# Optimization experiments

Hardware: AMD Instinct MI355X
Metric: run time of the kernel (lower is better)

## Reference

```python
import jax, jax.numpy as jnp
import numpy as np

S, B, DIN = 3, 4096, 1024
H1, H2, H3, D = 512, 384, 256, 128
K, C = 512, 3            # codebook size, n_codebooks
TEMP = 0.1               # contrastive temperature
EPS = 1e-12


def setup_inputs() -> dict:
    key = jax.random.key(0)
    ks = jax.random.split(key, 16)
    g = lambda k, shp, s=0.05: (jax.random.normal(k, shp, dtype=jnp.float32) * s)
    return {
        'x': jax.random.normal(ks[0], (S, B, DIN), dtype=jnp.float32),
        'enc_w1': g(ks[1], (S, DIN, H1)), 'enc_b1': g(ks[2], (S, H1)),
        'enc_w2': g(ks[3], (S, H1, H2)), 'enc_b2': g(ks[4], (S, H2)),
        'enc_w3': g(ks[5], (S, H2, H3)), 'enc_b3': g(ks[6], (S, H3)),
        'enc_w4': g(ks[7], (S, H3, D)),  'enc_b4': g(ks[8], (S, D)),
        'q_w1': g(ks[9], (D, D)), 'q_b1': g(ks[10], (D,)),
        'q_w2': g(ks[11], (D,)),
        'codebooks': jax.random.normal(ks[12], (C, K, D), dtype=jnp.float32),
    }


def _normalize(v):
    return v / jnp.maximum(jnp.linalg.norm(v, axis=-1, keepdims=True), EPS)


def _forward(x, enc_w1, enc_b1, enc_w2, enc_b2, enc_w3, enc_b3,
             enc_w4, enc_b4, q_w1, q_b1, q_w2, codebooks):
    sg = jax.lax.stop_gradient
    # per-source MLP encoders (stacked over source axis s)
    h = jax.nn.relu(jnp.einsum('sbi,sio->sbo', x, enc_w1) + enc_b1[:, None, :])
    h = jax.nn.relu(jnp.einsum('sbi,sio->sbo', h, enc_w2) + enc_b2[:, None, :])
    h = jax.nn.relu(jnp.einsum('sbi,sio->sbo', h, enc_w3) + enc_b3[:, None, :])
    emb = jnp.einsum('sbi,sio->sbo', h, enc_w4) + enc_b4[:, None, :]  # [S,B,D]

    # attention fusion: Linear->Tanh->Linear(1) per source, softmax over sources
    score = jnp.einsum('sbd,d->sb', jnp.tanh(jnp.einsum('sbd,de->sbe', emb, q_w1) + q_b1), q_w2)
    weight = jax.nn.softmax(score.T, axis=-1)                # [B,S]
    fused = jnp.einsum('bs,sbd->bd', weight, emb)            # [B,D]

    # residual VQ over C codebooks (straight-through, MSE losses)
    res = fused
    q_sum = jnp.zeros_like(fused)
    commit_loss = jnp.float32(0.0)
    for k in range(C):
        e = codebooks[k]                                     # [K,D]
        d2 = (jnp.sum(res * res, axis=1, keepdims=True)
              - 2.0 * res @ e.T + jnp.sum(e * e, axis=1))    # [B,K]
        ids = jnp.argmin(d2, axis=1)
        q = e[ids]                                           # [B,D]
        commit_loss = commit_loss + jnp.mean((sg(q) - res) ** 2)
        q_st = res + sg(q - res)                             # straight-through
        q_sum = q_sum + q_st
        res = res - q_st

    # codebook regularizer: mean pairwise cosine gram of normalized codebooks
    cbn = _normalize(codebooks)
    codebook_loss = jnp.mean(jnp.einsum('mkd,mjd->mkj', cbn, cbn))

    # contrastive losses (projection = identity)
    z1 = _normalize(q_sum)                                   # [B,D]
    contrast = []
    for s in range(S):
        z2 = _normalize(emb[s])
        refl = jnp.exp((z1 @ z1.T) / TEMP)                   # [B,B]
        between = jnp.exp((z1 @ z2.T) / TEMP)
        pos = jnp.diagonal(between)
        denom = refl.sum(1) + between.sum(1) - jnp.diagonal(refl)
        contrast.append(jnp.mean(-jnp.log(pos / denom)))

    return jnp.stack([1.0 * codebook_loss, 0.0 * commit_loss] + contrast)


def reference(x, enc_w1, enc_b1, enc_w2, enc_b2, enc_w3, enc_b3,
              enc_w4, enc_b4, q_w1, q_b1, q_w2, codebooks):
    return _forward(x, enc_w1, enc_b1, enc_w2, enc_b2, enc_w3, enc_b3,
                    enc_w4, enc_b4, q_w1, q_b1, q_w2, codebooks)
```

## Files before the change

### kernel.cpp

```cpp
#include <hip/hip_runtime.h>
#include <hip/hip_bf16.h>

#define S_   3
#define B_   4096
#define DIN_ 1024
#define H1_  512
#define H2_  384
#define H3_  256
#define D_   128
#define K_   512
#define C_   3
#define INV_T 10.0f
#define EPS_  1e-12f
#define EXP10 22026.465794806718f

typedef float f32x4 __attribute__((ext_vector_type(4)));
typedef short bf16x8 __attribute__((ext_vector_type(8)));

__device__ __forceinline__ unsigned short f2bf(float f) {
  unsigned int u = __float_as_uint(f);
  u = (u + 0x7FFF + ((u >> 16) & 1)) >> 16;
  return (unsigned short)u;
}

__device__ __forceinline__ float waveReduceSum(float v) {
#pragma unroll
  for (int off = 32; off > 0; off >>= 1) v += __shfl_down(v, off, 64);
  return v;
}

__device__ __forceinline__ float waveXorSum(float v) {
#pragma unroll
  for (int off = 32; off > 0; off >>= 1) v += __shfl_xor(v, off, 64);
  return v;
}

__device__ __forceinline__ float blockReduceSum128(float v, float* sbuf) {
  v = waveReduceSum(v);
  if ((threadIdx.x & 63) == 0) sbuf[threadIdx.x >> 6] = v;
  __syncthreads();
  float r = sbuf[0] + sbuf[1];
  __syncthreads();
  return r;
}

__global__ __launch_bounds__(256) void cvt_bf16_kernel(const float* __restrict__ in,
                                                       unsigned short* __restrict__ out,
                                                       int n) {
  int i = (blockIdx.x * 256 + threadIdx.x) * 4;
  if (i < n) {
    float4 v = *(const float4*)(in + i);
    out[i + 0] = f2bf(v.x); out[i + 1] = f2bf(v.y);
    out[i + 2] = f2bf(v.z); out[i + 3] = f2bf(v.w);
  }
}

__global__ __launch_bounds__(256) void transpose_w_kernel(const float* __restrict__ W,
                                                          unsigned short* __restrict__ Wt,
                                                          int K, int N) {
  const int s = blockIdx.z;
  const int k0 = blockIdx.x * 32, n0 = blockIdx.y * 32;
  const int tx = threadIdx.x, ty = threadIdx.y;
  __shared__ float t[32][33];
  const float* Ws = W + (size_t)s * K * N;
  unsigned short* Wts = Wt + (size_t)s * N * K;
#pragma unroll
  for (int i = 0; i < 4; i++)
    t[ty + 8 * i][tx] = Ws[(size_t)(k0 + ty + 8 * i) * N + n0 + tx];
  __syncthreads();
#pragma unroll
  for (int i = 0; i < 4; i++)
    Wts[(size_t)(n0 + ty + 8 * i) * K + k0 + tx] = f2bf(t[tx][ty + 8 * i]);
}

__global__ __launch_bounds__(256) void gemm_lds_kernel(
    const unsigned short* __restrict__ A, const unsigned short* __restrict__ Wt,
    const float* __restrict__ bias, void* __restrict__ Y,
    int K, int N, int relu, int out_f32) {
  const int t = threadIdx.x;
  const int lane = t & 63;
  const int w = t >> 6;
  const int ln = lane & 15, q = lane >> 4;
  const int wm = w >> 1, wn = w & 1;
  const int n0 = blockIdx.x * 128;
  const int mblk = blockIdx.y;
  const int s = mblk >> 6;
  const int m0 = mblk * 64;

  const unsigned short* Ag = A + (size_t)m0 * K;
  const unsigned short* Bg = Wt + (size_t)s * N * K + (size_t)n0 * K;
  const float* bs = bias + (size_t)s * N;

  __shared__ unsigned short Asm[2 * 64 * 32];
  __shared__ unsigned short Bsm[2 * 128 * 32];

  const int arow0 = t >> 3, ak8 = t & 7;
  const int aL0 = (ak8 >> 2) * 2048 + arow0 * 32 + (ak8 & 3) * 8;
  const int bL0 = (ak8 >> 2) * 4096 + arow0 * 32 + (ak8 & 3) * 8;
  const size_t gA0 = (size_t)arow0 * K + ak8 * 8;

  bf16x8 ra0 = *(const bf16x8*)(Ag + gA0);
  bf16x8 ra1 = *(const bf16x8*)(Ag + gA0 + (size_t)32 * K);
  bf16x8 rb0 = *(const bf16x8*)(Bg + gA0);
  bf16x8 rb1 = *(const bf16x8*)(Bg + gA0 + (size_t)32 * K);
  bf16x8 rb2 = *(const bf16x8*)(Bg + gA0 + (size_t)64 * K);
  bf16x8 rb3 = *(const bf16x8*)(Bg + gA0 + (size_t)96 * K);

  f32x4 acc[2][4];
#pragma unroll
  for (int i = 0; i < 2; i++)
#pragma unroll
    for (int j = 0; j < 4; j++) acc[i][j] = (f32x4){0.f, 0.f, 0.f, 0.f};

  for (int k0 = 0; k0 < K; k0 += 64) {
    *(bf16x8*)&Asm[aL0] = ra0;
    *(bf16x8*)&Asm[aL0 + 1024] = ra1;
    *(bf16x8*)&Bsm[bL0] = rb0;
    *(bf16x8*)&Bsm[bL0 + 1024] = rb1;
    *(bf16x8*)&Bsm[bL0 + 2048] = rb2;
    *(bf16x8*)&Bsm[bL0 + 3072] = rb3;
    __syncthreads();
    if (k0 + 64 < K) {
      const size_t g = gA0 + k0 + 64;
      ra0 = *(const bf16x8*)(Ag + g);
      ra1 = *(const bf16x8*)(Ag + g + (size_t)32 * K);
      rb0 = *(const bf16x8*)(Bg + g);
      rb1 = *(const bf16x8*)(Bg + g + (size_t)32 * K);
      rb2 = *(const bf16x8*)(Bg + g + (size_t)64 * K);
      rb3 = *(const bf16x8*)(Bg + g + (size_t)96 * K);
    }
    bf16x8 af[2][2], bf[4][2];
#pragma unroll
    for (int ti = 0; ti < 2; ti++)
#pragma unroll
      for (int ksl = 0; ksl < 2; ksl++)
        af[ti][ksl] = *(const bf16x8*)&Asm[ksl * 2048 + (wm * 32 + ti * 16 + ln) * 32 + q * 8];
#pragma unroll
    for (int tj = 0; tj < 4; tj++)
#pragma unroll
      for (int ksl = 0; ksl < 2; ksl++)
        bf[tj][ksl] = *(const bf16x8*)&Bsm[ksl * 4096 + (wn * 64 + tj * 16 + ln) * 32 + q * 8];
#pragma unroll
    for (int ksl = 0; ksl < 2; ksl++)
#pragma unroll
      for (int ti = 0; ti < 2; ti++)
#pragma unroll
        for (int tj = 0; tj < 4; tj++)
          acc[ti][tj] = __builtin_amdgcn_mfma_f32_16x16x32_bf16(af[ti][ksl], bf[tj][ksl], acc[ti][tj], 0, 0, 0);
    __syncthreads();
  }

#pragma unroll
  for (int ti = 0; ti < 2; ti++)
#pragma unroll
    for (int tj = 0; tj < 4; tj++) {
      const int cc = n0 + wn * 64 + tj * 16 + ln;
      const float bv = bs[cc];
#pragma unroll
      for (int reg = 0; reg < 4; reg++) {
        const int r = m0 + wm * 32 + ti * 16 + q * 4 + reg;
        float v = acc[ti][tj][reg] + bv;
        if (relu) v = fmaxf(v, 0.0f);
        if (out_f32) ((float*)Y)[(size_t)r * N + cc] = v;
        else ((unsigned short*)Y)[(size_t)r * N + cc] = f2bf(v);
      }
    }
}

__global__ __launch_bounds__(256) void score_kernel(
    const float* __restrict__ emb, const float* __restrict__ qw1,
    const float* __restrict__ qb1, const float* __restrict__ qw2,
    float* __restrict__ score) {
  const int b0 = blockIdx.x * 4;
  const int t = threadIdx.x;
  const int g = t >> 7, d = t & 127;
  __shared__ float e[12][D_];
  __shared__ float red[4][6];
#pragma unroll
  for (int i = 0; i < 3; i++) {
    int idx = i * 512 + t * 2;
    int r = idx >> 7, dd = idx & 127;
    int s = r >> 2, bi = r & 3;
    *(float2*)&e[r][dd] = *(const float2*)(emb + ((size_t)(s * B_ + b0 + bi)) * D_ + dd);
  }
  __syncthreads();
  float acc[6] = {0.f, 0.f, 0.f, 0.f, 0.f, 0.f};
  for (int i = 0; i < D_; i++) {
    float w = qw1[i * D_ + d];
#pragma unroll
    for (int j = 0; j < 6; j++) acc[j] = fmaf(e[g * 6 + j][i], w, acc[j]);
  }
  const float qb = qb1[d], q2 = qw2[d];
  float val[6];
#pragma unroll
  for (int j = 0; j < 6; j++) val[j] = tanhf(acc[j] + qb) * q2;
  const int wave = t >> 6;
#pragma unroll
  for (int j = 0; j < 6; j++) {
    float v = waveReduceSum(val[j]);
    if ((t & 63) == 0) red[wave][j] = v;
  }
  __syncthreads();
  if (t < 12) {
    int gg = t / 6, j = t % 6;
    int r = gg * 6 + j;
    int s = r >> 2, bi = r & 3;
    score[s * B_ + b0 + bi] = red[2 * gg][j] + red[2 * gg + 1][j];
  }
}

__global__ __launch_bounds__(128) void fuse_kernel(
    const float* __restrict__ emb, const float* __restrict__ score,
    float* __restrict__ fused) {
  const int b = blockIdx.x, d = threadIdx.x;
  float s0 = score[0 * B_ + b], s1 = score[1 * B_ + b], s2 = score[2 * B_ + b];
  float mx = fmaxf(s0, fmaxf(s1, s2));
  float e0 = __expf(s0 - mx), e1 = __expf(s1 - mx), e2 = __expf(s2 - mx);
  float inv = 1.0f / (e0 + e1 + e2);
  fused[(long long)b * D_ + d] =
      e0 * inv * emb[(long long)(0 * B_ + b) * D_ + d] +
      e1 * inv * emb[(long long)(1 * B_ + b) * D_ + d] +
      e2 * inv * emb[(long long)(2 * B_ + b) * D_ + d];
}

__global__ __launch_bounds__(64) void cbnorm2_kernel(const float* __restrict__ cb,
                                                     float* __restrict__ cbn2) {
  const int r = blockIdx.x, lane = threadIdx.x;
  const float* row = cb + (long long)r * D_;
  float v0 = row[lane], v1 = row[lane + 64];
  float t = waveReduceSum(v0 * v0 + v1 * v1);
  if (lane == 0) cbn2[r] = t;
}

__global__ __launch_bounds__(512) void vq_mfma_kernel(
    const float* __restrict__ fused, const float* __restrict__ cb,
    const unsigned short* __restrict__ cbb, const float* __restrict__ cbn2,
    float* __restrict__ qsum) {
  const int r0 = blockIdx.x * 16;
  const int t = threadIdx.x;
  const int w = t >> 6, lane = t & 63;
  const int ln = lane & 15, q = lane >> 4;
  __shared__ float resv[16][D_];
  __shared__ unsigned short resb[16][D_];
  __shared__ float candd[8][16];
  __shared__ int candk[8][16];
  __shared__ int bestk[16];

  {
    int idx = t * 4;
    int r = idx >> 7, dd = idx & 127;
    float4 v = *(const float4*)(fused + (size_t)(r0 + r) * D_ + dd);
    *(float4*)&resv[r][dd] = v;
    resb[r][dd + 0] = f2bf(v.x); resb[r][dd + 1] = f2bf(v.y);
    resb[r][dd + 2] = f2bf(v.z); resb[r][dd + 3] = f2bf(v.w);
  }
  __syncthreads();

  for (int c = 0; c < C_; c++) {
    bf16x8 a[4];
#pragma unroll
    for (int ks = 0; ks < 4; ks++)
      a[ks] = *(const bf16x8*)&resb[ln][ks * 32 + q * 8];
    f32x4 acc[4];
#pragma unroll
    for (int tt = 0; tt < 4; tt++) acc[tt] = (f32x4){0.f, 0.f, 0.f, 0.f};
#pragma unroll
    for (int tt = 0; tt < 4; tt++) {
      const int n = w * 64 + tt * 16 + ln;
      const unsigned short* bp = cbb + ((size_t)c * K_ + n) * D_;
#pragma unroll
      for (int ks = 0; ks < 4; ks++) {
        bf16x8 b = *(const bf16x8*)(bp + ks * 32 + q * 8);
        acc[tt] = __builtin_amdgcn_mfma_f32_16x16x32_bf16(a[ks], b, acc[tt], 0, 0, 0);
      }
    }
    float bd[4]; int bk[4];
#pragma unroll
    for (int reg = 0; reg < 4; reg++) { bd[reg] = 3.4e38f; bk[reg] = 0x7fffffff; }
#pragma unroll
    for (int tt = 0; tt < 4; tt++) {
      const int col = w * 64 + tt * 16 + ln;
      const float n2 = cbn2[c * K_ + col];
#pragma unroll
      for (int reg = 0; reg < 4; reg++) {
        float dist = n2 - 2.0f * acc[tt][reg];
        if (dist < bd[reg] || (dist == bd[reg] && col < bk[reg])) { bd[reg] = dist; bk[reg] = col; }
      }
    }
#pragma unroll
    for (int reg = 0; reg < 4; reg++) {
#pragma unroll
      for (int off = 8; off > 0; off >>= 1) {
        float d1 = __shfl_down(bd[reg], off, 16);
        int k1 = __shfl_down(bk[reg], off, 16);
        if (d1 < bd[reg] || (d1 == bd[reg] && k1 < bk[reg])) { bd[reg] = d1; bk[reg] = k1; }
      }
      if (ln == 0) { candd[w][q * 4 + reg] = bd[reg]; candk[w][q * 4 + reg] = bk[reg]; }
    }
    __syncthreads();
    if (w == 0) {
      int row = lane >> 2, g = lane & 3;
      float d0 = candd[2 * g][row]; int k0 = candk[2 * g][row];
      float d1 = candd[2 * g + 1][row]; int k1 = candk[2 * g + 1][row];
      if (d1 < d0 || (d1 == d0 && k1 < k0)) { d0 = d1; k0 = k1; }
#pragma unroll
      for (int off = 2; off > 0; off >>= 1) {
        float dn = __shfl_down(d0, off, 4);
        int kn = __shfl_down(k0, off, 4);
        if (dn < d0 || (dn == d0 && kn < k0)) { d0 = dn; k0 = kn; }
      }
      if (g == 0) bestk[row] = k0;
    }
    __syncthreads();
    {
      int idx = t * 4;
      int r = idx >> 7, dd = idx & 127;
      const float4 qv = *(const float4*)(cb + ((size_t)c * K_ + bestk[r]) * D_ + dd);
      float4 rv = *(float4*)&resv[r][dd];
      rv.x -= qv.x; rv.y -= qv.y; rv.z -= qv.z; rv.w -= qv.w;
      *(float4*)&resv[r][dd] = rv;
      resb[r][dd + 0] = f2bf(rv.x); resb[r][dd + 1] = f2bf(rv.y);
      resb[r][dd + 2] = f2bf(rv.z); resb[r][dd + 3] = f2bf(rv.w);
    }
    __syncthreads();
  }

  {
    int idx = t * 4;
    int r = idx >> 7, dd = idx & 127;
    float4 f = *(const float4*)(fused + (size_t)(r0 + r) * D_ + dd);
    float4 rv = *(float4*)&resv[r][dd];
    f.x -= rv.x; f.y -= rv.y; f.z -= rv.z; f.w -= rv.w;
    *(float4*)(qsum + (size_t)(r0 + r) * D_ + dd) = f;
  }
}

__global__ __launch_bounds__(256) void normalize_kernel(
    const float* __restrict__ qsum, const float* __restrict__ emb,
    float* __restrict__ z, unsigned short* __restrict__ zb) {
  const int g = blockIdx.x * 4 + (threadIdx.x >> 6);
  const int lane = threadIdx.x & 63;
  const float* src = (g < B_) ? (qsum + (size_t)g * D_) : (emb + (size_t)(g - B_) * D_);
  float2 v = *(const float2*)(src + lane * 2);
  float n2 = waveXorSum(v.x * v.x + v.y * v.y);
  float inv = 1.0f / fmaxf(sqrtf(n2), EPS_);
  float zx = v.x * inv, zy = v.y * inv;
  *(float2*)(z + (size_t)g * D_ + lane * 2) = make_float2(zx, zy);
  zb[(size_t)g * D_ + lane * 2 + 0] = f2bf(zx);
  zb[(size_t)g * D_ + lane * 2 + 1] = f2bf(zy);
}

__global__ __launch_bounds__(256) void contrast_mfma_kernel(
    const unsigned short* __restrict__ zb, float* __restrict__ rsP) {
  const int jc = blockIdx.x, ib = blockIdx.y, m = blockIdx.z;
  const int t = threadIdx.x;
  const int w = t >> 6, lane = t & 63;
  const int ln = lane & 15, q = lane >> 4;
  const int i0 = ib * 128 + w * 32;
  const unsigned short* Za = zb;
  const unsigned short* Zm = zb + (size_t)m * B_ * D_;

  __shared__ unsigned short Zsm[64 * 136];

  bf16x8 a[2][4];
#pragma unroll
  for (int si = 0; si < 2; si++)
#pragma unroll
    for (int ks = 0; ks < 4; ks++)
      a[si][ks] = *(const bf16x8*)(Za + (size_t)(i0 + si * 16 + ln) * D_ + ks * 32 + q * 8);

  const unsigned short* tb = Zm + (size_t)(jc * 1024) * D_;
  bf16x8 rz[4];
#pragma unroll
  for (int p = 0; p < 4; p++)
    rz[p] = *(const bf16x8*)(tb + t * 8 + p * 2048);

  float e[2][4] = {};
  for (int jt = 0; jt < 16; jt++) {
#pragma unroll
    for (int p = 0; p < 4; p++) {
      int c = t + p * 256;
      *(bf16x8*)&Zsm[(c >> 4) * 136 + (c & 15) * 8] = rz[p];
    }
    __syncthreads();
    if (jt + 1 < 16) {
      const unsigned short* tn = Zm + (size_t)(jc * 1024 + (jt + 1) * 64) * D_;
#pragma unroll
      for (int p = 0; p < 4; p++)
        rz[p] = *(const bf16x8*)(tn + t * 8 + p * 2048);
    }
    f32x4 acc[2][4];
#pragma unroll
    for (int si = 0; si < 2; si++)
#pragma unroll
      for (int tj = 0; tj < 4; tj++) acc[si][tj] = (f32x4){0.f, 0.f, 0.f, 0.f};
#pragma unroll
    for (int tj = 0; tj < 4; tj++) {
      bf16x8 b[4];
#pragma unroll
      for (int ks = 0; ks < 4; ks++)
        b[ks] = *(const bf16x8*)&Zsm[(tj * 16 + ln) * 136 + ks * 32 + q * 8];
#pragma unroll
      for (int ks = 0; ks < 4; ks++) {
        acc[0][tj] = __builtin_amdgcn_mfma_f32_16x16x32_bf16(a[0][ks], b[ks], acc[0][tj], 0, 0, 0);
        acc[1][tj] = __builtin_amdgcn_mfma_f32_16x16x32_bf16(a[1][ks], b[ks], acc[1][tj], 0, 0, 0);
      }
    }
#pragma unroll
    for (int si = 0; si < 2; si++)
#pragma unroll
      for (int reg = 0; reg < 4; reg++) {
        float s = 0.f;
#pragma unroll
        for (int tj = 0; tj < 4; tj++) s += __expf(acc[si][tj][reg] * INV_T);
        e[si][reg] += s;
      }
    __syncthreads();
  }
#pragma unroll
  for (int si = 0; si < 2; si++)
#pragma unroll
    for (int reg = 0; reg < 4; reg++) {
#pragma unroll
      for (int off = 8; off > 0; off >>= 1)
        e[si][reg] += __shfl_xor(e[si][reg], off, 16);
    }
  if (ln == 0) {
#pragma unroll
    for (int si = 0; si < 2; si++)
#pragma unroll
      for (int reg = 0; reg < 4; reg++)
        rsP[((size_t)m * 4 + jc) * B_ + i0 + si * 16 + q * 4 + reg] = e[si][reg];
  }
}

__global__ __launch_bounds__(256) void pos_kernel(const float* __restrict__ z,
                                                  float* __restrict__ pos) {
  const int p = blockIdx.x * 4 + (threadIdx.x >> 6);
  const int lane = threadIdx.x & 63;
  const int s = p >> 12, b = p & (B_ - 1);
  float2 v1 = *(const float2*)(z + (size_t)b * D_ + lane * 2);
  float2 v2 = *(const float2*)(z + (size_t)((1 + s) * B_ + b) * D_ + lane * 2);
  float t = waveXorSum(v1.x * v2.x + v1.y * v2.y);
  if (lane == 0) pos[s * B_ + b] = t;
}

__global__ __launch_bounds__(128) void cbsum_kernel(const float* __restrict__ cb,
                                                    const float* __restrict__ cbn2,
                                                    float* __restrict__ cbsum) {
  const int m = blockIdx.x >> 3;
  const int k0 = (blockIdx.x & 7) * 64;
  const int d = threadIdx.x;
  float acc = 0.0f;
  for (int k = k0; k < k0 + 64; k++) {
    float inv = 1.0f / fmaxf(sqrtf(cbn2[m * K_ + k]), EPS_);
    acc += cb[((size_t)m * K_ + k) * D_ + d] * inv;
  }
  atomicAdd(&cbsum[m * D_ + d], acc);
}

__global__ __launch_bounds__(256) void lossred_kernel(const float* __restrict__ rsP,
                                                      const float* __restrict__ pos,
                                                      float* __restrict__ loss_acc) {
  const int s = blockIdx.y;
  const int i = blockIdx.x * 256 + threadIdx.x;
  __shared__ float red[4];
  float denom = -EXP10;
#pragma unroll
  for (int jc = 0; jc < 4; jc++) {
    denom += rsP[(size_t)jc * B_ + i];
    denom += rsP[((size_t)(1 + s) * 4 + jc) * B_ + i];
  }
  float val = logf(denom) - pos[s * B_ + i] * INV_T;
  float v = waveReduceSum(val);
  if ((threadIdx.x & 63) == 0) red[threadIdx.x >> 6] = v;
  __syncthreads();
  if (threadIdx.x == 0) atomicAdd(&loss_acc[s], red[0] + red[1] + red[2] + red[3]);
}

__global__ __launch_bounds__(128) void finalize_kernel(const float* __restrict__ cbsum,
                                                       const float* __restrict__ loss_acc,
                                                       float* __restrict__ out) {
  const int d = threadIdx.x;
  __shared__ float red[2];
  float acc = 0.0f;
#pragma unroll
  for (int m = 0; m < C_; m++) {
    float v = cbsum[m * D_ + d];
    acc += v * v;
  }
  float tot = blockReduceSum128(acc, red);
  if (d == 0) out[0] = tot * (1.0f / (3.0f * 512.0f * 512.0f));
  if (d == 1) out[1] = 0.0f;
  if (d >= 2 && d < 5) out[d] = loss_acc[d - 2] * (1.0f / 4096.0f);
}

extern "C" void kernel_launch(void* const* d_in, const int* in_sizes, int n_in,
                              void* d_out, int out_size, void* d_ws, size_t ws_size,
                              hipStream_t stream) {
  const float* x    = (const float*)d_in[0];
  const float* w1   = (const float*)d_in[1];
  const float* b1   = (const float*)d_in[2];
  const float* w2   = (const float*)d_in[3];
  const float* b2   = (const float*)d_in[4];
  const float* w3   = (const float*)d_in[5];
  const float* b3   = (const float*)d_in[6];
  const float* w4   = (const float*)d_in[7];
  const float* b4   = (const float*)d_in[8];
  const float* qw1  = (const float*)d_in[9];
  const float* qb1  = (const float*)d_in[10];
  const float* qw2  = (const float*)d_in[11];
  const float* cb   = (const float*)d_in[12];
  float* out = (float*)d_out;
  char* base = (char*)d_ws;

  size_t o = 0;
  auto alloc = [&](size_t bytes) { size_t r = o; o += (bytes + 255) & ~(size_t)255; return r; };
  size_t o_xb   = alloc((size_t)S_ * B_ * DIN_ * 2);
  size_t o_wt1  = alloc((size_t)S_ * H1_ * DIN_ * 2);
  size_t o_wt2  = alloc((size_t)S_ * H2_ * H1_ * 2);
  size_t o_wt3  = alloc((size_t)S_ * H3_ * H2_ * 2);
  size_t o_wt4  = alloc((size_t)S_ * D_ * H3_ * 2);
  size_t o_h1b  = alloc((size_t)S_ * B_ * H1_ * 2);
  size_t o_h2b  = alloc((size_t)S_ * B_ * H2_ * 2);
  size_t o_h3b  = alloc((size_t)S_ * B_ * H3_ * 2);
  size_t o_emb  = alloc((size_t)S_ * B_ * D_ * 4);
  size_t o_scr  = alloc((size_t)S_ * B_ * 4);
  size_t o_fus  = alloc((size_t)B_ * D_ * 4);
  size_t o_qs   = alloc((size_t)B_ * D_ * 4);
  size_t o_z    = alloc((size_t)4 * B_ * D_ * 4);
  size_t o_zb   = alloc((size_t)4 * B_ * D_ * 2);
  size_t o_cbn2 = alloc((size_t)C_ * K_ * 4);
  size_t o_cbb  = alloc((size_t)C_ * K_ * D_ * 2);
  size_t o_rsP  = alloc((size_t)4 * 4 * B_ * 4);
  size_t o_lacc = alloc(64);
  size_t o_cbs  = alloc((size_t)C_ * D_ * 4);
  size_t o_pos  = alloc((size_t)S_ * B_ * 4);
  (void)ws_size; (void)in_sizes; (void)n_in; (void)out_size;

  unsigned short* xb  = (unsigned short*)(base + o_xb);
  unsigned short* wt1 = (unsigned short*)(base + o_wt1);
  unsigned short* wt2 = (unsigned short*)(base + o_wt2);
  unsigned short* wt3 = (unsigned short*)(base + o_wt3);
  unsigned short* wt4 = (unsigned short*)(base + o_wt4);
  unsigned short* h1b = (unsigned short*)(base + o_h1b);
  unsigned short* h2b = (unsigned short*)(base + o_h2b);
  unsigned short* h3b = (unsigned short*)(base + o_h3b);
  float* emb   = (float*)(base + o_emb);
  float* score = (float*)(base + o_scr);
  float* fused = (float*)(base + o_fus);
  float* qsum  = (float*)(base + o_qs);
  float* z     = (float*)(base + o_z);
  unsigned short* zb = (unsigned short*)(base + o_zb);
  float* cbn2  = (float*)(base + o_cbn2);
  unsigned short* cbb = (unsigned short*)(base + o_cbb);
  float* rsP   = (float*)(base + o_rsP);
  float* lacc  = (float*)(base + o_lacc);
  float* cbsum = (float*)(base + o_cbs);
  float* pos   = (float*)(base + o_pos);

  hipMemsetAsync(lacc, 0, 64, stream);
  hipMemsetAsync(cbsum, 0, (size_t)C_ * D_ * 4, stream);

  cvt_bf16_kernel<<<dim3((S_ * B_ * DIN_) / 1024), 256, 0, stream>>>(x, xb, S_ * B_ * DIN_);
  cvt_bf16_kernel<<<dim3((C_ * K_ * D_) / 1024), 256, 0, stream>>>(cb, cbb, C_ * K_ * D_);
  transpose_w_kernel<<<dim3(DIN_ / 32, H1_ / 32, S_), dim3(32, 8), 0, stream>>>(w1, wt1, DIN_, H1_);
  transpose_w_kernel<<<dim3(H1_ / 32, H2_ / 32, S_), dim3(32, 8), 0, stream>>>(w2, wt2, H1_, H2_);
  transpose_w_kernel<<<dim3(H2_ / 32, H3_ / 32, S_), dim3(32, 8), 0, stream>>>(w3, wt3, H2_, H3_);
  transpose_w_kernel<<<dim3(H3_ / 32, D_ / 32, S_), dim3(32, 8), 0, stream>>>(w4, wt4, H3_, D_);

  const int Mtot = S_ * B_;
  gemm_lds_kernel<<<dim3(H1_ / 128, Mtot / 64), 256, 0, stream>>>(xb, wt1, b1, h1b, DIN_, H1_, 1, 0);
  gemm_lds_kernel<<<dim3(H2_ / 128, Mtot / 64), 256, 0, stream>>>(h1b, wt2, b2, h2b, H1_, H2_, 1, 0);
  gemm_lds_kernel<<<dim3(H3_ / 128, Mtot / 64), 256, 0, stream>>>(h2b, wt3, b3, h3b, H2_, H3_, 1, 0);
  gemm_lds_kernel<<<dim3(D_ / 128, Mtot / 64), 256, 0, stream>>>(h3b, wt4, b4, emb, H3_, D_, 0, 1);

  score_kernel<<<dim3(B_ / 4), 256, 0, stream>>>(emb, qw1, qb1, qw2, score);
  fuse_kernel<<<dim3(B_), 128, 0, stream>>>(emb, score, fused);

  cbnorm2_kernel<<<dim3(C_ * K_), 64, 0, stream>>>(cb, cbn2);
  vq_mfma_kernel<<<dim3(B_ / 16), 512, 0, stream>>>(fused, cb, cbb, cbn2, qsum);

  normalize_kernel<<<dim3(4 * B_ / 4), 256, 0, stream>>>(qsum, emb, z, zb);

  contrast_mfma_kernel<<<dim3(4, 32, 4), 256, 0, stream>>>(zb, rsP);
  pos_kernel<<<dim3(S_ * B_ / 4), 256, 0, stream>>>(z, pos);

  cbsum_kernel<<<dim3(C_ * 8), 128, 0, stream>>>(cb, cbn2, cbsum);

  lossred_kernel<<<dim3(B_ / 256, S_), 256, 0, stream>>>(rsP, pos, lacc);

  finalize_kernel<<<dim3(1), 128, 0, stream>>>(cbsum, lacc, out);
}
```

Measured before the change: 270.6 us.

## Fuse small kernels and replace atomics with partial-sum buffers

Merges score and fuse into one kernel that reuses the embeddings already staged in shared memory, merges normalize and pos into one per-row kernel, and combines the codebook norm and codebook sum computations. The atomic accumulators and their memsets are replaced by per-block partial sums that the finalize kernel reduces. The fp32 z buffer is dropped. The aim is fewer launches and less global traffic, at the cost of some under-occupied fused kernels.

```diff
diff --git a/kernel.cpp b/kernel.cpp
--- a/kernel.cpp
+++ b/kernel.cpp
@@ -167,15 +167,16 @@
     }
 }
 
-__global__ __launch_bounds__(256) void score_kernel(
+__global__ __launch_bounds__(256) void score_fuse_kernel(
     const float* __restrict__ emb, const float* __restrict__ qw1,
     const float* __restrict__ qb1, const float* __restrict__ qw2,
-    float* __restrict__ score) {
+    float* __restrict__ fused) {
   const int b0 = blockIdx.x * 4;
   const int t = threadIdx.x;
   const int g = t >> 7, d = t & 127;
   __shared__ float e[12][D_];
   __shared__ float red[4][6];
+  __shared__ float sc[12];
 #pragma unroll
   for (int i = 0; i < 3; i++) {
     int idx = i * 512 + t * 2;
@@ -203,33 +204,46 @@
   __syncthreads();
   if (t < 12) {
     int gg = t / 6, j = t % 6;
-    int r = gg * 6 + j;
-    int s = r >> 2, bi = r & 3;
-    score[s * B_ + b0 + bi] = red[2 * gg][j] + red[2 * gg + 1][j];
-  }
-}
-
-__global__ __launch_bounds__(128) void fuse_kernel(
-    const float* __restrict__ emb, const float* __restrict__ score,
-    float* __restrict__ fused) {
-  const int b = blockIdx.x, d = threadIdx.x;
-  float s0 = score[0 * B_ + b], s1 = score[1 * B_ + b], s2 = score[2 * B_ + b];
-  float mx = fmaxf(s0, fmaxf(s1, s2));
-  float e0 = __expf(s0 - mx), e1 = __expf(s1 - mx), e2 = __expf(s2 - mx);
-  float inv = 1.0f / (e0 + e1 + e2);
-  fused[(long long)b * D_ + d] =
-      e0 * inv * emb[(long long)(0 * B_ + b) * D_ + d] +
-      e1 * inv * emb[(long long)(1 * B_ + b) * D_ + d] +
-      e2 * inv * emb[(long long)(2 * B_ + b) * D_ + d];
-}
-
-__global__ __launch_bounds__(64) void cbnorm2_kernel(const float* __restrict__ cb,
-                                                     float* __restrict__ cbn2) {
-  const int r = blockIdx.x, lane = threadIdx.x;
-  const float* row = cb + (long long)r * D_;
-  float v0 = row[lane], v1 = row[lane + 64];
-  float t = waveReduceSum(v0 * v0 + v1 * v1);
-  if (lane == 0) cbn2[r] = t;
+    sc[gg * 6 + j] = red[2 * gg][j] + red[2 * gg + 1][j];
+  }
+  __syncthreads();
+#pragma unroll
+  for (int p = 0; p < 2; p++) {
+    int idx = p * 256 + t;
+    int bi = idx >> 7, dd = idx & 127;
+    float s0 = sc[bi], s1 = sc[4 + bi], s2 = sc[8 + bi];
+    float mx = fmaxf(s0, fmaxf(s1, s2));
+    float e0 = __expf(s0 - mx), e1 = __expf(s1 - mx), e2 = __expf(s2 - mx);
+    float inv = 1.0f / (e0 + e1 + e2);
+    fused[(size_t)(b0 + bi) * D_ + dd] =
+        (e0 * e[bi][dd] + e1 * e[4 + bi][dd] + e2 * e[8 + bi][dd]) * inv;
+  }
+}
+
+__global__ __launch_bounds__(512) void cbns_kernel(const float* __restrict__ cb,
+                                                   float* __restrict__ cbn2,
+                                                   float* __restrict__ cbsumP) {
+  const int m = blockIdx.x >> 3;
+  const int k0 = (blockIdx.x & 7) * 64;
+  const int t = threadIdx.x, w = t >> 6, lane = t & 63;
+  __shared__ float invn[64];
+#pragma unroll
+  for (int r = w * 8; r < w * 8 + 8; r++) {
+    int k = k0 + r;
+    float2 v = *(const float2*)(cb + ((size_t)m * K_ + k) * D_ + lane * 2);
+    float n2 = waveXorSum(v.x * v.x + v.y * v.y);
+    if (lane == 0) {
+      cbn2[m * K_ + k] = n2;
+      invn[r] = 1.0f / fmaxf(sqrtf(n2), EPS_);
+    }
+  }
+  __syncthreads();
+  if (t < D_) {
+    float acc = 0.0f;
+    for (int r = 0; r < 64; r++)
+      acc += cb[((size_t)m * K_ + k0 + r) * D_ + t] * invn[r];
+    cbsumP[(size_t)blockIdx.x * D_ + t] = acc;
+  }
 }
 
 __global__ __launch_bounds__(512) void vq_mfma_kernel(
@@ -335,19 +349,28 @@
   }
 }
 
-__global__ __launch_bounds__(256) void normalize_kernel(
+__global__ __launch_bounds__(256) void normpos_kernel(
     const float* __restrict__ qsum, const float* __restrict__ emb,
-    float* __restrict__ z, unsigned short* __restrict__ zb) {
-  const int g = blockIdx.x * 4 + (threadIdx.x >> 6);
-  const int lane = threadIdx.x & 63;
-  const float* src = (g < B_) ? (qsum + (size_t)g * D_) : (emb + (size_t)(g - B_) * D_);
+    unsigned short* __restrict__ zb, float* __restrict__ pos) {
+  const int b = blockIdx.x;
+  const int w = threadIdx.x >> 6, lane = threadIdx.x & 63;
+  __shared__ float zl[4][D_];
+  const float* src = (w == 0) ? (qsum + (size_t)b * D_)
+                              : (emb + (size_t)((w - 1) * B_ + b) * D_);
   float2 v = *(const float2*)(src + lane * 2);
   float n2 = waveXorSum(v.x * v.x + v.y * v.y);
   float inv = 1.0f / fmaxf(sqrtf(n2), EPS_);
   float zx = v.x * inv, zy = v.y * inv;
-  *(float2*)(z + (size_t)g * D_ + lane * 2) = make_float2(zx, zy);
-  zb[(size_t)g * D_ + lane * 2 + 0] = f2bf(zx);
-  zb[(size_t)g * D_ + lane * 2 + 1] = f2bf(zy);
+  const size_t g = (size_t)w * B_ + b;
+  zb[g * D_ + lane * 2 + 0] = f2bf(zx);
+  zb[g * D_ + lane * 2 + 1] = f2bf(zy);
+  zl[w][lane * 2] = zx; zl[w][lane * 2 + 1] = zy;
+  __syncthreads();
+  if (w >= 1) {
+    float2 a = *(const float2*)&zl[0][lane * 2];
+    float dsum = waveXorSum(a.x * zx + a.y * zy);
+    if (lane == 0) pos[(w - 1) * B_ + b] = dsum;
+  }
 }
 
 __global__ __launch_bounds__(256) void contrast_mfma_kernel(
@@ -434,34 +457,9 @@
   }
 }
 
-__global__ __launch_bounds__(256) void pos_kernel(const float* __restrict__ z,
-                                                  float* __restrict__ pos) {
-  const int p = blockIdx.x * 4 + (threadIdx.x >> 6);
-  const int lane = threadIdx.x & 63;
-  const int s = p >> 12, b = p & (B_ - 1);
-  float2 v1 = *(const float2*)(z + (size_t)b * D_ + lane * 2);
-  float2 v2 = *(const float2*)(z + (size_t)((1 + s) * B_ + b) * D_ + lane * 2);
-  float t = waveXorSum(v1.x * v2.x + v1.y * v2.y);
-  if (lane == 0) pos[s * B_ + b] = t;
-}
-
-__global__ __launch_bounds__(128) void cbsum_kernel(const float* __restrict__ cb,
-                                                    const float* __restrict__ cbn2,
-                                                    float* __restrict__ cbsum) {
-  const int m = blockIdx.x >> 3;
-  const int k0 = (blockIdx.x & 7) * 64;
-  const int d = threadIdx.x;
-  float acc = 0.0f;
-  for (int k = k0; k < k0 + 64; k++) {
-    float inv = 1.0f / fmaxf(sqrtf(cbn2[m * K_ + k]), EPS_);
-    acc += cb[((size_t)m * K_ + k) * D_ + d] * inv;
-  }
-  atomicAdd(&cbsum[m * D_ + d], acc);
-}
-
 __global__ __launch_bounds__(256) void lossred_kernel(const float* __restrict__ rsP,
                                                       const float* __restrict__ pos,
-                                                      float* __restrict__ loss_acc) {
+                                                      float* __restrict__ lossP) {
   const int s = blockIdx.y;
   const int i = blockIdx.x * 256 + threadIdx.x;
   __shared__ float red[4];
@@ -475,24 +473,32 @@
   float v = waveReduceSum(val);
   if ((threadIdx.x & 63) == 0) red[threadIdx.x >> 6] = v;
   __syncthreads();
-  if (threadIdx.x == 0) atomicAdd(&loss_acc[s], red[0] + red[1] + red[2] + red[3]);
-}
-
-__global__ __launch_bounds__(128) void finalize_kernel(const float* __restrict__ cbsum,
-                                                       const float* __restrict__ loss_acc,
+  if (threadIdx.x == 0)
+    lossP[s * 16 + blockIdx.x] = red[0] + red[1] + red[2] + red[3];
+}
+
+__global__ __launch_bounds__(128) void finalize_kernel(const float* __restrict__ cbsumP,
+                                                       const float* __restrict__ lossP,
                                                        float* __restrict__ out) {
   const int d = threadIdx.x;
   __shared__ float red[2];
   float acc = 0.0f;
 #pragma unroll
   for (int m = 0; m < C_; m++) {
-    float v = cbsum[m * D_ + d];
+    float v = 0.0f;
+#pragma unroll
+    for (int blk = 0; blk < 8; blk++) v += cbsumP[(size_t)(m * 8 + blk) * D_ + d];
     acc += v * v;
   }
   float tot = blockReduceSum128(acc, red);
   if (d == 0) out[0] = tot * (1.0f / (3.0f * 512.0f * 512.0f));
   if (d == 1) out[1] = 0.0f;
-  if (d >= 2 && d < 5) out[d] = loss_acc[d - 2] * (1.0f / 4096.0f);
+  if (d >= 2 && d < 5) {
+    float l = 0.0f;
+#pragma unroll
+    for (int x = 0; x < 16; x++) l += lossP[(d - 2) * 16 + x];
+    out[d] = l * (1.0f / 4096.0f);
+  }
 }
 
 extern "C" void kernel_launch(void* const* d_in, const int* in_sizes, int n_in,
@@ -525,16 +531,14 @@
   size_t o_h2b  = alloc((size_t)S_ * B_ * H2_ * 2);
   size_t o_h3b  = alloc((size_t)S_ * B_ * H3_ * 2);
   size_t o_emb  = alloc((size_t)S_ * B_ * D_ * 4);
-  size_t o_scr  = alloc((size_t)S_ * B_ * 4);
   size_t o_fus  = alloc((size_t)B_ * D_ * 4);
   size_t o_qs   = alloc((size_t)B_ * D_ * 4);
-  size_t o_z    = alloc((size_t)4 * B_ * D_ * 4);
   size_t o_zb   = alloc((size_t)4 * B_ * D_ * 2);
   size_t o_cbn2 = alloc((size_t)C_ * K_ * 4);
   size_t o_cbb  = alloc((size_t)C_ * K_ * D_ * 2);
   size_t o_rsP  = alloc((size_t)4 * 4 * B_ * 4);
-  size_t o_lacc = alloc(64);
-  size_t o_cbs  = alloc((size_t)C_ * D_ * 4);
+  size_t o_cbsP = alloc((size_t)C_ * 8 * D_ * 4);
+  size_t o_lossP= alloc((size_t)S_ * 16 * 4);
   size_t o_pos  = alloc((size_t)S_ * B_ * 4);
   (void)ws_size; (void)in_sizes; (void)n_in; (void)out_size;
 
@@ -547,20 +551,15 @@
   unsigned short* h2b = (unsigned short*)(base + o_h2b);
   unsigned short* h3b = (unsigned short*)(base + o_h3b);
   float* emb   = (float*)(base + o_emb);
-  float* score = (float*)(base + o_scr);
   float* fused = (float*)(base + o_fus);
   float* qsum  = (float*)(base + o_qs);
-  float* z     = (float*)(base + o_z);
   unsigned short* zb = (unsigned short*)(base + o_zb);
   float* cbn2  = (float*)(base + o_cbn2);
   unsigned short* cbb = (unsigned short*)(base + o_cbb);
   float* rsP   = (float*)(base + o_rsP);
-  float* lacc  = (float*)(base + o_lacc);
-  float* cbsum = (float*)(base + o_cbs);
+  float* cbsumP= (float*)(base + o_cbsP);
+  float* lossP = (float*)(base + o_lossP);
   float* pos   = (float*)(base + o_pos);
-
-  hipMemsetAsync(lacc, 0, 64, stream);
-  hipMemsetAsync(cbsum, 0, (size_t)C_ * D_ * 4, stream);
 
   cvt_bf16_kernel<<<dim3((S_ * B_ * DIN_) / 1024), 256, 0, stream>>>(x, xb, S_ * B_ * DIN_);
   cvt_bf16_kernel<<<dim3((C_ * K_ * D_) / 1024), 256, 0, stream>>>(cb, cbb, C_ * K_ * D_);
@@ -569,26 +568,23 @@
   transpose_w_kernel<<<dim3(H2_ / 32, H3_ / 32, S_), dim3(32, 8), 0, stream>>>(w3, wt3, H2_, H3_);
   transpose_w_kernel<<<dim3(H3_ / 32, D_ / 32, S_), dim3(32, 8), 0, stream>>>(w4, wt4, H3_, D_);
 
+  cbns_kernel<<<dim3(C_ * 8), 512, 0, stream>>>(cb, cbn2, cbsumP);
+
   const int Mtot = S_ * B_;
   gemm_lds_kernel<<<dim3(H1_ / 128, Mtot / 64), 256, 0, stream>>>(xb, wt1, b1, h1b, DIN_, H1_, 1, 0);
   gemm_lds_kernel<<<dim3(H2_ / 128, Mtot / 64), 256, 0, stream>>>(h1b, wt2, b2, h2b, H1_, H2_, 1, 0);
   gemm_lds_kernel<<<dim3(H3_ / 128, Mtot / 64), 256, 0, stream>>>(h2b, wt3, b3, h3b, H2_, H3_, 1, 0);
   gemm_lds_kernel<<<dim3(D_ / 128, Mtot / 64), 256, 0, stream>>>(h3b, wt4, b4, emb, H3_, D_, 0, 1);
 
-  score_kernel<<<dim3(B_ / 4), 256, 0, stream>>>(emb, qw1, qb1, qw2, score);
-  fuse_kernel<<<dim3(B_), 128, 0, stream>>>(emb, score, fused);
-
-  cbnorm2_kernel<<<dim3(C_ * K_), 64, 0, stream>>>(cb, cbn2);
+  score_fuse_kernel<<<dim3(B_ / 4), 256, 0, stream>>>(emb, qw1, qb1, qw2, fused);
+
   vq_mfma_kernel<<<dim3(B_ / 16), 512, 0, stream>>>(fused, cb, cbb, cbn2, qsum);
 
-  normalize_kernel<<<dim3(4 * B_ / 4), 256, 0, stream>>>(qsum, emb, z, zb);
+  normpos_kernel<<<dim3(B_), 256, 0, stream>>>(qsum, emb, zb, pos);
 
   contrast_mfma_kernel<<<dim3(4, 32, 4), 256, 0, stream>>>(zb, rsP);
-  pos_kernel<<<dim3(S_ * B_ / 4), 256, 0, stream>>>(z, pos);
-
-  cbsum_kernel<<<dim3(C_ * 8), 128, 0, stream>>>(cb, cbn2, cbsum);
-
-  lossred_kernel<<<dim3(B_ / 256, S_), 256, 0, stream>>>(rsP, pos, lacc);
-
-  finalize_kernel<<<dim3(1), 128, 0, stream>>>(cbsum, lacc, out);
-}
+
+  lossred_kernel<<<dim3(B_ / 256, S_), 256, 0, stream>>>(rsP, pos, lossP);
+
+  finalize_kernel<<<dim3(1), 128, 0, stream>>>(cbsumP, lossP, out);
+}
```

After: 257.9 us. -4.7%, faster.
